# Kernel tuning notes

Measured on AMD Instinct MI355X. Metric: run time of the kernel, lower is better.

The kernel has to match this reference:

```python
import jax, jax.numpy as jnp
import numpy as np

N = 64            # HiPPO order
DT = 1.0 / 512.0  # discretization timestep ~ 1/seq_len


def _hippo_legt_discrete(n, dt):
    """Continuous HiPPO-LegT (A,B) then bilinear (Tustin) discretization,
    matching scipy.signal.cont2discrete(..., method='bilinear')."""
    Q = np.arange(n, dtype=np.float64)
    R = (2 * Q + 1)[:, None]
    j, i = np.meshgrid(Q, Q)
    A = np.where(i < j, -1.0, (-1.0) ** (i - j + 1)) * R
    B = (-1.0) ** Q[:, None] * R  # (n, 1)
    I = np.eye(n)
    ima = I - (dt / 2.0) * A
    Ad = np.linalg.solve(ima, I + (dt / 2.0) * A)
    Bd = np.linalg.solve(ima, dt * B).squeeze(-1)  # (n,)
    return Ad, Bd


def setup_inputs() -> dict:
    key = jax.random.key(0)
    inputs = jax.random.normal(key, (16, 128, 512), dtype=jnp.float32)  # (b, d, L)
    Ad, Bd = _hippo_legt_discrete(N, DT)
    return {
        "inputs": inputs,
        "A": jnp.asarray(Ad, dtype=jnp.float32),  # (N, N)
        "B": jnp.asarray(Bd, dtype=jnp.float32),  # (N,)
    }


def reference(inputs, A, B):
    # inputs: (b, d, L) -> iterate over last axis, state c: (b, d, N)
    fs = jnp.moveaxis(inputs, -1, 0)  # (L, b, d)
    c0 = jnp.zeros(inputs.shape[:-1] + (A.shape[0],), dtype=inputs.dtype)

    def step(c, f):
        # c_t = c_{t-1} @ A^T + f_t[..., None] * B   (F.linear(c, A) == c @ A^T)
        c_new = c @ A.T + f[..., None] * B
        return c_new, c_new

    _, cs = jax.lax.scan(step, c0, fs)
    return cs  # (L, b, d, N)
```

## Files before the change

### kernel.cpp

```cpp
#include <hip/hip_runtime.h>


typedef _Float16 half8  __attribute__((ext_vector_type(8)));
typedef float    f32x4  __attribute__((ext_vector_type(4)));

#define SEQN 2048
#define LT   512

typedef const __attribute__((address_space(1))) unsigned int kGU32;
typedef __attribute__((address_space(3))) unsigned int kLU32;

__device__ __forceinline__ void cp16(const void* g, void* l) {
  __builtin_amdgcn_global_load_lds((kGU32*)g, (kLU32*)l, 16, 0, 0);
}

__device__ __forceinline__ void mul64(const float* XT, const float* Y,
                                      float* outT, float* outN, int t) {
  const int r = (t >> 5) * 4;
  const int c = (t & 31) * 2;
  float a00 = 0.f, a01 = 0.f, a10 = 0.f, a11 = 0.f;
  float a20 = 0.f, a21 = 0.f, a30 = 0.f, a31 = 0.f;
#pragma unroll 4
  for (int l = 0; l < 64; ++l) {
    const float4 x = *(const float4*)(XT + l * 64 + r);
    const float2 y = *(const float2*)(Y + l * 64 + c);
    a00 += x.x * y.x; a01 += x.x * y.y;
    a10 += x.y * y.x; a11 += x.y * y.y;
    a20 += x.z * y.x; a21 += x.z * y.y;
    a30 += x.w * y.x; a31 += x.w * y.y;
  }
  __syncthreads();
  if (outT) {
    outT[(c + 0) * 64 + r + 0] = a00; outT[(c + 1) * 64 + r + 0] = a01;
    outT[(c + 0) * 64 + r + 1] = a10; outT[(c + 1) * 64 + r + 1] = a11;
    outT[(c + 0) * 64 + r + 2] = a20; outT[(c + 1) * 64 + r + 2] = a21;
    outT[(c + 0) * 64 + r + 3] = a30; outT[(c + 1) * 64 + r + 3] = a31;
  }
  if (outN) {
    outN[(r + 0) * 64 + c + 0] = a00; outN[(r + 0) * 64 + c + 1] = a01;
    outN[(r + 1) * 64 + c + 0] = a10; outN[(r + 1) * 64 + c + 1] = a11;
    outN[(r + 2) * 64 + c + 0] = a20; outN[(r + 2) * 64 + c + 1] = a21;
    outN[(r + 3) * 64 + c + 0] = a30; outN[(r + 3) * 64 + c + 1] = a31;
  }
  __syncthreads();
}

__global__ __launch_bounds__(512) void squares_fh(
    const float* __restrict__ A, const float* __restrict__ f,
    float* __restrict__ SqT, _Float16* __restrict__ fh) {
  __shared__ float S[4096];
  __shared__ float STr[4096];
  const int t = threadIdx.x;
  if (blockIdx.x == 0) {
    for (int i = t; i < 4096; i += 512) {
      const float v = A[i];
      S[i] = v;
      STr[(i & 63) * 64 + (i >> 6)] = v;
    }
    __syncthreads();
    for (int i = t; i < 4096; i += 512) SqT[i] = STr[i];
    for (int k = 1; k < 9; ++k) {
      mul64(STr, S, STr, S, t);
      for (int i = t; i < 4096; i += 512) SqT[k * 4096 + i] = STr[i];
    }
  } else {
    const size_t g = (size_t)(blockIdx.x - 1) * 512 + t;
    const float4* s = (const float4*)(f + g * 8);
    const float4 a = s[0], b = s[1];
    half8 v;
    v[0] = (_Float16)a.x; v[1] = (_Float16)a.y;
    v[2] = (_Float16)a.z; v[3] = (_Float16)a.w;
    v[4] = (_Float16)b.x; v[5] = (_Float16)b.y;
    v[6] = (_Float16)b.z; v[7] = (_Float16)b.w;
    *(half8*)(fh + g * 8) = v;
  }
}

__global__ __launch_bounds__(512) void kvec_fill(
    const float* __restrict__ SqT, const float* __restrict__ B,
    _Float16* __restrict__ Lc) {
  __shared__ float Kb[8][64];
  const int t = threadIdx.x;
  const int b = blockIdx.x;

  {
    const int ch = b * 512 + t;
    const int c = ch >> 12, n = (ch >> 6) & 63, zc = ch & 63;
    const uint4 zz = {0u, 0u, 0u, 0u};
    *(uint4*)(Lc + (size_t)c * 65536 + n * 1024 + 512 + zc * 8) = zz;
  }
  if (b == 0) {
    for (int e = t; e < 1792; e += 512) {
      int e2 = e, c = 1;
      while (e2 >= 64 * c) { e2 -= 64 * c; ++c; }
      const int n = e2 & 63, dz = e2 >> 6;
      Lc[(size_t)c * 65536 + n * 1024 + (512 - c + dz)] = (_Float16)0.f;
    }
  }

  const int g = t >> 6, n = t & 63;
  const int i = b * 8 + g;
  float kreg = B[n];
  for (int k = 0; k < 9; ++k) {
    Kb[g][n] = kreg;
    __syncthreads();
    if ((i >> k) & 1) {
      const float* Sk = SqT + k * 4096 + n;
      float s = 0.f;
#pragma unroll 16
      for (int m = 0; m < 64; ++m) s += Sk[m * 64] * Kb[g][m];
      kreg = s;
    }
    __syncthreads();
  }
#pragma unroll
  for (int c = 0; c < 8; ++c) {
    const int z = 511 - i - c;
    if (z >= 0) Lc[(size_t)c * 65536 + n * 1024 + z] = (_Float16)kreg;
  }
}

__global__ __launch_bounds__(256, 4) void causal_gemm(
    const _Float16* __restrict__ fh, const _Float16* __restrict__ Lc,
    float* __restrict__ out) {
  __shared__ _Float16 Xs[128 * 64];
  __shared__ _Float16 Ws[128 * 64];

  const int tid = threadIdx.x;
  const int bn = 255 - (int)blockIdx.x;
  const int bm = blockIdx.y;
  const int lane = tid & 63, wid = tid >> 6;
  const int wm = wid >> 1, wn = wid & 1;
  const int l15 = lane & 15, quad = lane >> 4;
  const int KH = (2 * bn + 65) >> 6;

  const int srow = lane >> 3;
  const int jp = (lane & 7) ^ srow;

  const _Float16* xp[4];
  const _Float16* wp[4];
  int ldso[4];
#pragma unroll
  for (int q = 0; q < 4; ++q) {
    const int rl = wid * 32 + q * 8 + srow;
    xp[q] = fh + (size_t)(bm * 128 + rl) * LT + jp * 8;
    const int tau = 2 * bn + (rl >> 6);
    const int n = rl & 63;
    const int o0 = 511 - tau;
    const int c = o0 & 7;
    wp[q] = Lc + (size_t)c * 65536 + n * 1024 + (o0 - c) + jp * 8;
    ldso[q] = (wid * 32 + q * 8) * 64;
  }

  f32x4 acc[4][4];
  const f32x4 z4 = {0.f, 0.f, 0.f, 0.f};
#pragma unroll
  for (int i = 0; i < 4; ++i)
#pragma unroll
    for (int j = 0; j < 4; ++j) acc[i][j] = z4;

  for (int kh = 0; kh < KH; ++kh) {
    if (kh) __syncthreads();
    const size_t go = (size_t)kh * 64;
#pragma unroll
    for (int q = 0; q < 4; ++q) {
      cp16(xp[q] + go, &Xs[ldso[q]]);
      cp16(wp[q] + go, &Ws[ldso[q]]);
    }
    __syncthreads();

#pragma unroll
    for (int kk = 0; kk < 2; ++kk) {
      half8 av[4], bv[4];
#pragma unroll
      for (int fm = 0; fm < 4; ++fm) {
        const int r = wm * 64 + fm * 16 + l15;
        av[fm] =
            *(const half8*)&Xs[r * 64 + (((kk * 4 + quad) ^ (l15 & 7)) << 3)];
      }
#pragma unroll
      for (int fn = 0; fn < 4; ++fn) {
        const int r = wn * 64 + fn * 16 + l15;
        bv[fn] =
            *(const half8*)&Ws[r * 64 + (((kk * 4 + quad) ^ (l15 & 7)) << 3)];
      }
#pragma unroll
      for (int fm = 0; fm < 4; ++fm)
#pragma unroll
        for (int fn = 0; fn < 4; ++fn)
          acc[fm][fn] = __builtin_amdgcn_mfma_f32_16x16x32_f16(
              av[fm], bv[fn], acc[fm][fn], 0, 0, 0);
    }
  }

  const int taug = bn * 2 + wn;
#pragma unroll
  for (int fm = 0; fm < 4; ++fm) {
#pragma unroll
    for (int rr = 0; rr < 4; ++rr) {
      const size_t row =
          (size_t)taug * SEQN + (bm * 128 + wm * 64 + fm * 16 + quad * 4 + rr);
      float* o = out + row * 64 + l15;
#pragma unroll
      for (int fn = 0; fn < 4; ++fn) o[fn * 16] = acc[fm][fn][rr];
    }
  }
}

extern "C" void kernel_launch(void* const* d_in, const int* in_sizes, int n_in,
                              void* d_out, int out_size, void* d_ws,
                              size_t ws_size, hipStream_t stream) {
  const float* f = (const float*)d_in[0];
  const float* A = (const float*)d_in[1];
  const float* B = (const float*)d_in[2];
  float* out = (float*)d_out;

  _Float16* Lc = (_Float16*)d_ws;
  float* SqT = (float*)((char*)d_ws + (1 << 20));
  _Float16* fh =
      (_Float16*)((char*)d_ws + (1 << 20) + (192 << 10));

  squares_fh<<<257, 512, 0, stream>>>(A, f, SqT, fh);
  kvec_fill<<<64, 512, 0, stream>>>(SqT, B, Lc);
  causal_gemm<<<dim3(256, 16), 256, 0, stream>>>(fh, Lc, out);
}
```

Before: 325.5 us.

## Pre-tile f16 inputs into MFMA fragment layout and load A operand directly from global

The f32-to-f16 conversion now writes the input into a tiled layout that matches the MFMA A-fragment, so the GEMM can read A operands straight from global memory into registers instead of staging them through LDS. This halves LDS use and traffic per block, and the launch bound no longer forces four blocks per CU. It also skips the 32-wide k sub-steps that lie beyond the causal bound. The trade-off is that A fragments become uncached global loads issued in the inner loop, which can expose latency.

```diff
diff --git a/kernel.cpp b/kernel.cpp
--- a/kernel.cpp
+++ b/kernel.cpp
@@ -47,7 +47,7 @@
 
 __global__ __launch_bounds__(512) void squares_fh(
     const float* __restrict__ A, const float* __restrict__ f,
-    float* __restrict__ SqT, _Float16* __restrict__ fh) {
+    float* __restrict__ SqT, _Float16* __restrict__ fh_t) {
   __shared__ float S[4096];
   __shared__ float STr[4096];
   const int t = threadIdx.x;
@@ -64,15 +64,18 @@
       for (int i = t; i < 4096; i += 512) SqT[k * 4096 + i] = STr[i];
     }
   } else {
-    const size_t g = (size_t)(blockIdx.x - 1) * 512 + t;
-    const float4* s = (const float4*)(f + g * 8);
+    const int g = (blockIdx.x - 1) * 512 + t;
+    const int row = g >> 6, kc = g & 63;
+    const float4* s = (const float4*)(f + (size_t)row * LT + kc * 8);
     const float4 a = s[0], b = s[1];
     half8 v;
     v[0] = (_Float16)a.x; v[1] = (_Float16)a.y;
     v[2] = (_Float16)a.z; v[3] = (_Float16)a.w;
     v[4] = (_Float16)b.x; v[5] = (_Float16)b.y;
     v[6] = (_Float16)b.z; v[7] = (_Float16)b.w;
-    *(half8*)(fh + g * 8) = v;
+    const int off = ((row >> 4) * 16 + (kc >> 2)) * 512 + (row & 15) * 32 +
+                    (kc & 3) * 8;
+    *(half8*)(fh_t + off) = v;
   }
 }
 
@@ -120,10 +123,9 @@
   }
 }
 
-__global__ __launch_bounds__(256, 4) void causal_gemm(
-    const _Float16* __restrict__ fh, const _Float16* __restrict__ Lc,
+__global__ __launch_bounds__(256) void causal_gemm(
+    const _Float16* __restrict__ fh_t, const _Float16* __restrict__ Lc,
     float* __restrict__ out) {
-  __shared__ _Float16 Xs[128 * 64];
   __shared__ _Float16 Ws[128 * 64];
 
   const int tid = threadIdx.x;
@@ -132,18 +134,17 @@
   const int lane = tid & 63, wid = tid >> 6;
   const int wm = wid >> 1, wn = wid & 1;
   const int l15 = lane & 15, quad = lane >> 4;
-  const int KH = (2 * bn + 65) >> 6;
+  const int needK = 2 * bn + 2;
+  const int KH = (needK + 63) >> 6;
 
   const int srow = lane >> 3;
   const int jp = (lane & 7) ^ srow;
 
-  const _Float16* xp[4];
   const _Float16* wp[4];
   int ldso[4];
 #pragma unroll
   for (int q = 0; q < 4; ++q) {
     const int rl = wid * 32 + q * 8 + srow;
-    xp[q] = fh + (size_t)(bm * 128 + rl) * LT + jp * 8;
     const int tau = 2 * bn + (rl >> 6);
     const int n = rl & 63;
     const int o0 = 511 - tau;
@@ -152,6 +153,9 @@
     ldso[q] = (wid * 32 + q * 8) * 64;
   }
 
+  const _Float16* px =
+      fh_t + (size_t)(bm * 8 + wm * 4) * 8192 + l15 * 32 + quad * 8;
+
   f32x4 acc[4][4];
   const f32x4 z4 = {0.f, 0.f, 0.f, 0.f};
 #pragma unroll
@@ -163,33 +167,29 @@
     if (kh) __syncthreads();
     const size_t go = (size_t)kh * 64;
 #pragma unroll
-    for (int q = 0; q < 4; ++q) {
-      cp16(xp[q] + go, &Xs[ldso[q]]);
-      cp16(wp[q] + go, &Ws[ldso[q]]);
-    }
+    for (int q = 0; q < 4; ++q) cp16(wp[q] + go, &Ws[ldso[q]]);
     __syncthreads();
 
 #pragma unroll
     for (int kk = 0; kk < 2; ++kk) {
-      half8 av[4], bv[4];
-#pragma unroll
-      for (int fm = 0; fm < 4; ++fm) {
-        const int r = wm * 64 + fm * 16 + l15;
-        av[fm] =
-            *(const half8*)&Xs[r * 64 + (((kk * 4 + quad) ^ (l15 & 7)) << 3)];
+      if (kh * 64 + kk * 32 < needK) {
+        half8 av[4], bv[4];
+#pragma unroll
+        for (int fm = 0; fm < 4; ++fm)
+          av[fm] = *(const half8*)(px + fm * 8192 + (kh * 2 + kk) * 512);
+#pragma unroll
+        for (int fn = 0; fn < 4; ++fn) {
+          const int r = wn * 64 + fn * 16 + l15;
+          bv[fn] = *(const half8*)&Ws[r * 64 +
+                                      (((kk * 4 + quad) ^ (l15 & 7)) << 3)];
+        }
+#pragma unroll
+        for (int fm = 0; fm < 4; ++fm)
+#pragma unroll
+          for (int fn = 0; fn < 4; ++fn)
+            acc[fm][fn] = __builtin_amdgcn_mfma_f32_16x16x32_f16(
+                av[fm], bv[fn], acc[fm][fn], 0, 0, 0);
       }
-#pragma unroll
-      for (int fn = 0; fn < 4; ++fn) {
-        const int r = wn * 64 + fn * 16 + l15;
-        bv[fn] =
-            *(const half8*)&Ws[r * 64 + (((kk * 4 + quad) ^ (l15 & 7)) << 3)];
-      }
-#pragma unroll
-      for (int fm = 0; fm < 4; ++fm)
-#pragma unroll
-        for (int fn = 0; fn < 4; ++fn)
-          acc[fm][fn] = __builtin_amdgcn_mfma_f32_16x16x32_f16(
-              av[fm], bv[fn], acc[fm][fn], 0, 0, 0);
     }
   }
 
@@ -217,10 +217,10 @@
 
   _Float16* Lc = (_Float16*)d_ws;
   float* SqT = (float*)((char*)d_ws + (1 << 20));
-  _Float16* fh =
+  _Float16* fh_t =
       (_Float16*)((char*)d_ws + (1 << 20) + (192 << 10));
 
-  squares_fh<<<257, 512, 0, stream>>>(A, f, SqT, fh);
+  squares_fh<<<257, 512, 0, stream>>>(A, f, SqT, fh_t);
   kvec_fill<<<64, 512, 0, stream>>>(SqT, B, Lc);
-  causal_gemm<<<dim3(256, 16), 256, 0, stream>>>(fh, Lc, out);
-}
+  causal_gemm<<<dim3(256, 16), 256, 0, stream>>>(fh_t, Lc, out);
+}
```

New measurement: 326.4 us. Within noise of the previous version (+0.3%).
